# Performance work log

Measured on AMD Instinct MI355X. Metric: run time of the kernel, lower is better.

## Reference

```python
import jax, jax.numpy as jnp
import numpy as np

N_NODES = 50000
N_EDGES = 800000
IN_FEATS = 96
HIDDEN = 96
OUT_FEATS = 8


def setup_inputs() -> dict:
    key = jax.random.key(0)
    k = jax.random.split(key, 10)
    features = jax.random.normal(k[0], (N_NODES, IN_FEATS), dtype=jnp.float32)
    src = jax.random.randint(k[1], (N_EDGES,), 0, N_NODES, dtype=jnp.int32)
    dst = jax.random.randint(k[2], (N_EDGES,), 0, N_NODES, dtype=jnp.int32)
    # DGL GraphConv weights: shape (in, out), xavier-uniform; bias zeros (we use small randn for nontrivial grads)
    def glorot(kk, fan_in, fan_out):
        lim = np.sqrt(6.0 / (fan_in + fan_out))
        return jax.random.uniform(kk, (fan_in, fan_out), jnp.float32, -lim, lim)
    W1 = glorot(k[3], IN_FEATS, HIDDEN)
    b1 = jnp.zeros((HIDDEN,), jnp.float32)
    W2 = glorot(k[4], HIDDEN, HIDDEN)
    b2 = jnp.zeros((HIDDEN,), jnp.float32)
    # torch Linear readout: weight [out, in], bias [out]
    Wr = glorot(k[5], OUT_FEATS, HIDDEN)
    br = jnp.zeros((OUT_FEATS,), jnp.float32)
    return {"features": features, "src": src, "dst": dst,
            "W1": W1, "b1": b1, "W2": W2, "b2": b2, "Wr": Wr, "br": br}


def _degree_norms(src, dst, n_nodes):
    ones = jnp.ones(src.shape[0], jnp.float32)
    deg_out = jax.ops.segment_sum(ones, src, num_segments=n_nodes)
    deg_in = jax.ops.segment_sum(ones, dst, num_segments=n_nodes)
    norm_out = jnp.clip(deg_out, 1.0, None) ** -0.5  # D_out^{-1/2}
    norm_in = jnp.clip(deg_in, 1.0, None) ** -0.5    # D_in^{-1/2}
    return norm_out, norm_in


def _graph_conv(x, src, dst, norm_out, norm_in, W, b):
    # DGL GraphConv, norm='both': scale src feats, sum-aggregate over edges,
    # scale by in-degree norm, dense transform + bias.
    x = x * norm_out[:, None]
    msgs = x[src]                                           # [E, d] gather
    agg = jax.ops.segment_sum(msgs, dst, num_segments=x.shape[0])  # [N, d] scatter-add
    agg = agg * norm_in[:, None]
    return agg @ W + b


def reference(features, src, dst, W1, b1, W2, b2, Wr, br):
    n = features.shape[0]
    norm_out, norm_in = _degree_norms(src, dst, n)
    x = jax.nn.relu(_graph_conv(features, src, dst, norm_out, norm_in, W1, b1))
    x = _graph_conv(x, src, dst, norm_out, norm_in, W2, b2)
    hg = jnp.mean(x, axis=0, keepdims=True)  # [1, hidden]
    return hg @ Wr.T + br                    # [1, out_feats]
```

## Files before the change

### kernel.cpp

```cpp
#include <hip/hip_runtime.h>


constexpr int NN = 50000;
constexpr int NE = 800000;
constexpr int NB = 196;
constexpr int CAP = 6144;

constexpr int OFF_SVEC     = 0;
constexpr int OFF_BCURD    = 256;
constexpr int OFF_BCURS    = 3392;
constexpr int OFF_NORM_OUT = 6528;
constexpr int OFF_NORM_IN  = 56528;
constexpr int OFF_CW       = 106528;
constexpr int OFF_ROW_PTR  = 156528;
constexpr int OFF_EDGE_SRC = 206532;
constexpr int OFF_PD       = 606532;
constexpr int OFF_PS       = 1810756;
constexpr int OFF_YP       = 606532;
constexpr size_t ZERO_BYTES = (size_t)(OFF_NORM_OUT) * 4;

__global__ __launch_bounds__(256)
void k_part(const int* __restrict__ src, const int* __restrict__ dst,
            int* __restrict__ bcur_d, int* __restrict__ bcur_s,
            int* __restrict__ pd, int* __restrict__ ps) {
  __shared__ int hd[256], hs[256], cd[256], cs[256];
  const int t = threadIdx.x;
  hd[t] = 0; hs[t] = 0;
  __syncthreads();
  const int e0 = blockIdx.x * 2048;
  int s_[8], d_[8];
#pragma unroll
  for (int i = 0; i < 8; ++i) {
    int e = e0 + i * 256 + t;
    bool v = e < NE;
    s_[i] = v ? src[e] : -1;
    d_[i] = v ? dst[e] : -1;
    if (v) { atomicAdd(&hd[d_[i] >> 8], 1); atomicAdd(&hs[s_[i] >> 8], 1); }
  }
  __syncthreads();
  if (t < NB) {
    int c = hd[t];
    cd[t] = c ? (t * CAP + atomicAdd(&bcur_d[t * 16], c)) : 0;
    c = hs[t];
    cs[t] = c ? (t * CAP + atomicAdd(&bcur_s[t * 16], c)) : 0;
  }
  __syncthreads();
#pragma unroll
  for (int i = 0; i < 8; ++i) {
    if (s_[i] >= 0) {
      int pos = atomicAdd(&cd[d_[i] >> 8], 1);
      pd[pos] = (s_[i] << 8) | (d_[i] & 255);
      int pos2 = atomicAdd(&cs[s_[i] >> 8], 1);
      ps[pos2] = (d_[i] << 8) | (s_[i] & 255);
    }
  }
}

__global__ __launch_bounds__(256)
void k_csr(const int* __restrict__ pd, const int* __restrict__ bcur_d,
           int* __restrict__ row_ptr, float* __restrict__ norm_in,
           unsigned short* __restrict__ edge_src) {
  __shared__ int hist[256], cur[256], sc[256];
  const int t = threadIdx.x, b = blockIdx.x;
  hist[t] = 0;
  __syncthreads();
  const int cnt = bcur_d[b * 16];
  const int* pe = pd + b * CAP;
  for (int i = t; i < cnt; i += 256) atomicAdd(&hist[pe[i] & 255], 1);

  sc[t] = (t < b) ? bcur_d[t * 16] : 0;
  __syncthreads();
  for (int s = 128; s > 0; s >>= 1) {
    if (t < s) sc[t] += sc[t + s];
    __syncthreads();
  }
  const int base0 = sc[0];
  __syncthreads();

  int h = hist[t];
  sc[t] = h;
  __syncthreads();
  for (int off = 1; off < 256; off <<= 1) {
    int u = (t >= off) ? sc[t - off] : 0;
    __syncthreads();
    sc[t] += u;
    __syncthreads();
  }
  int excl = base0 + sc[t] - h;
  int n = b * 256 + t;
  if (n < NN) {
    row_ptr[n] = excl;
    norm_in[n] = 1.0f / sqrtf((float)max(h, 1));
  }
  cur[t] = excl;
  __syncthreads();
  if (b == NB - 1 && t == 0) row_ptr[NN] = base0 + cnt;

  for (int i = t; i < cnt; i += 256) {
    int p = pe[i];
    int pos = atomicAdd(&cur[p & 255], 1);
    edge_src[pos] = (unsigned short)(p >> 8);
  }
}

__global__ __launch_bounds__(256)
void k_bin_src(const int* __restrict__ ps, const int* __restrict__ bcur_s,
               const float* __restrict__ norm_in,
               float* __restrict__ norm_out, float* __restrict__ cw) {
  __shared__ int dout[256];
  __shared__ float craw[256];
  const int t = threadIdx.x, b = blockIdx.x;
  dout[t] = 0; craw[t] = 0.f;
  __syncthreads();
  const int cnt = bcur_s[b * 16];
  const int* pe = ps + b * CAP;
  for (int i = t; i < cnt; i += 256) {
    int p = pe[i];
    atomicAdd(&dout[p & 255], 1);
    atomicAdd(&craw[p & 255], norm_in[p >> 8]);
  }
  __syncthreads();
  int n = b * 256 + t;
  if (n < NN) {
    float no = 1.0f / sqrtf((float)max(dout[t], 1));
    norm_out[n] = no;
    cw[n] = no * craw[t];
  }
}

__global__ __launch_bounds__(256, 6)
void k_xform(const float* __restrict__ feats, const float* __restrict__ norm_out,
             const float* __restrict__ W1, float* __restrict__ YP) {
  __shared__ float XT[96][68];
  const int t = threadIdx.x;
  const int nb = blockIdx.x * 64;

  const float4* f4 = (const float4*)feats;
#pragma unroll
  for (int i = 0; i < 6; ++i) {
    int idx4 = i * 256 + t;
    int n = idx4 / 24;
    int kq = idx4 % 24;
    int ng = nb + n;
    float4 v = make_float4(0.f, 0.f, 0.f, 0.f);
    float no = 0.f;
    if (ng < NN) { v = f4[(size_t)ng * 24 + kq]; no = norm_out[ng]; }
    XT[kq * 4 + 0][n] = v.x * no;
    XT[kq * 4 + 1][n] = v.y * no;
    XT[kq * 4 + 2][n] = v.z * no;
    XT[kq * 4 + 3][n] = v.w * no;
  }
  __syncthreads();

  const int tn = t & 7;
  const int tm = t >> 3;
  float acc0[12], acc1[12];
#pragma unroll
  for (int c = 0; c < 12; ++c) { acc0[c] = 0.f; acc1[c] = 0.f; }

  const float4* W4 = (const float4*)(W1 + 12 * tn);
#pragma unroll 4
  for (int k = 0; k < 96; ++k) {
    float2 x = *(const float2*)&XT[k][2 * tm];
    float4 w0 = W4[k * 24 + 0];
    float4 w1 = W4[k * 24 + 1];
    float4 w2 = W4[k * 24 + 2];
    const float w[12] = {w0.x, w0.y, w0.z, w0.w, w1.x, w1.y, w1.z, w1.w,
                         w2.x, w2.y, w2.z, w2.w};
#pragma unroll
    for (int c = 0; c < 12; ++c) {
      acc0[c] = fmaf(x.x, w[c], acc0[c]);
      acc1[c] = fmaf(x.y, w[c], acc1[c]);
    }
  }

  int n0 = nb + 2 * tm;
  if (n0 < NN) {
    float4* yp = (float4*)(YP + ((size_t)tn * NN + n0) * 12);
    yp[0] = make_float4(acc0[0], acc0[1], acc0[2], acc0[3]);
    yp[1] = make_float4(acc0[4], acc0[5], acc0[6], acc0[7]);
    yp[2] = make_float4(acc0[8], acc0[9], acc0[10], acc0[11]);
  }
  if (n0 + 1 < NN) {
    float4* yp = (float4*)(YP + ((size_t)tn * NN + n0 + 1) * 12);
    yp[0] = make_float4(acc1[0], acc1[1], acc1[2], acc1[3]);
    yp[1] = make_float4(acc1[4], acc1[5], acc1[6], acc1[7]);
    yp[2] = make_float4(acc1[8], acc1[9], acc1[10], acc1[11]);
  }
}

__global__ __launch_bounds__(256, 6)
void k_agg(const float* __restrict__ YP,
           const float* __restrict__ norm_in, const float* __restrict__ cw,
           const int* __restrict__ row_ptr, const unsigned short* __restrict__ edge_src,
           const float* __restrict__ b1, float* __restrict__ svec) {
  __shared__ float red[12];
  const int tid = threadIdx.x;
  if (tid < 12) red[tid] = 0.f;
  __syncthreads();

  const int panel = blockIdx.x & 7;
  const int bp    = blockIdx.x >> 3;
  const int g = tid >> 5, l = tid & 31;
  const int ei = l / 3;
  const int q  = l - 3 * ei;
  const bool act = (l < 24);

  const float* Yp = YP + (size_t)panel * NN * 12;
  float4 b4 = make_float4(0.f, 0.f, 0.f, 0.f);
  if (l < 3) b4 = ((const float4*)b1)[3 * panel + l];

  float a0 = 0.f, a1 = 0.f, a2 = 0.f, a3 = 0.f;

  const int gid = bp * 8 + g;
  for (int n = gid; n < NN; n += 4096) {
    const int m = n + 2048;
    const bool hb = (m < NN);
    int e1a = row_ptr[n + 1], basea = row_ptr[n];
    int e1b = 0, baseb = 0;
    if (hb) { e1b = row_ptr[m + 1]; baseb = row_ptr[m]; }
    float va0 = 0.f, va1 = 0.f, va2 = 0.f, va3 = 0.f;
    float vb0 = 0.f, vb1 = 0.f, vb2 = 0.f, vb3 = 0.f;

    while (basea < e1a || baseb < e1b) {
      int cnta = min(32, e1a - basea);
      int cntb = min(32, e1b - baseb);
      int esa = 0, esb = 0;
      if (basea + l < e1a) esa = edge_src[basea + l];
      if (baseb + l < e1b) esb = edge_src[baseb + l];

      if (cnta > 0) {
        int s0 = __shfl(esa, ei, 32);
        float4 f0 = make_float4(0.f, 0.f, 0.f, 0.f);
        if (act && ei < cnta) f0 = *(const float4*)(Yp + (size_t)s0 * 12 + 4 * q);
        if (cnta > 8) {
          int s1 = __shfl(esa, 8 + ei, 32);
          float4 f1 = make_float4(0.f, 0.f, 0.f, 0.f);
          if (act && 8 + ei < cnta) f1 = *(const float4*)(Yp + (size_t)s1 * 12 + 4 * q);
          f0.x += f1.x; f0.y += f1.y; f0.z += f1.z; f0.w += f1.w;
        }
        if (cnta > 16) {
          int s2 = __shfl(esa, 16 + ei, 32);
          int s3 = __shfl(esa, 24 + ei, 32);
          float4 f2 = make_float4(0.f, 0.f, 0.f, 0.f), f3 = f2;
          if (act && 16 + ei < cnta) f2 = *(const float4*)(Yp + (size_t)s2 * 12 + 4 * q);
          if (act && 24 + ei < cnta) f3 = *(const float4*)(Yp + (size_t)s3 * 12 + 4 * q);
          f0.x += f2.x + f3.x; f0.y += f2.y + f3.y;
          f0.z += f2.z + f3.z; f0.w += f2.w + f3.w;
        }
        va0 += f0.x; va1 += f0.y; va2 += f0.z; va3 += f0.w;
      }
      if (cntb > 0) {
        int s0 = __shfl(esb, ei, 32);
        float4 f0 = make_float4(0.f, 0.f, 0.f, 0.f);
        if (act && ei < cntb) f0 = *(const float4*)(Yp + (size_t)s0 * 12 + 4 * q);
        if (cntb > 8) {
          int s1 = __shfl(esb, 8 + ei, 32);
          float4 f1 = make_float4(0.f, 0.f, 0.f, 0.f);
          if (act && 8 + ei < cntb) f1 = *(const float4*)(Yp + (size_t)s1 * 12 + 4 * q);
          f0.x += f1.x; f0.y += f1.y; f0.z += f1.z; f0.w += f1.w;
        }
        if (cntb > 16) {
          int s2 = __shfl(esb, 16 + ei, 32);
          int s3 = __shfl(esb, 24 + ei, 32);
          float4 f2 = make_float4(0.f, 0.f, 0.f, 0.f), f3 = f2;
          if (act && 16 + ei < cntb) f2 = *(const float4*)(Yp + (size_t)s2 * 12 + 4 * q);
          if (act && 24 + ei < cntb) f3 = *(const float4*)(Yp + (size_t)s3 * 12 + 4 * q);
          f0.x += f2.x + f3.x; f0.y += f2.y + f3.y;
          f0.z += f2.z + f3.z; f0.w += f2.w + f3.w;
        }
        vb0 += f0.x; vb1 += f0.y; vb2 += f0.z; vb3 += f0.w;
      }
      basea += 32; baseb += 32;
    }

    va0 += __shfl(va0, l + 12, 32); va1 += __shfl(va1, l + 12, 32);
    va2 += __shfl(va2, l + 12, 32); va3 += __shfl(va3, l + 12, 32);
    va0 += __shfl(va0, l + 6, 32);  va1 += __shfl(va1, l + 6, 32);
    va2 += __shfl(va2, l + 6, 32);  va3 += __shfl(va3, l + 6, 32);
    va0 += __shfl(va0, l + 3, 32);  va1 += __shfl(va1, l + 3, 32);
    va2 += __shfl(va2, l + 3, 32);  va3 += __shfl(va3, l + 3, 32);

    vb0 += __shfl(vb0, l + 12, 32); vb1 += __shfl(vb1, l + 12, 32);
    vb2 += __shfl(vb2, l + 12, 32); vb3 += __shfl(vb3, l + 12, 32);
    vb0 += __shfl(vb0, l + 6, 32);  vb1 += __shfl(vb1, l + 6, 32);
    vb2 += __shfl(vb2, l + 6, 32);  vb3 += __shfl(vb3, l + 6, 32);
    vb0 += __shfl(vb0, l + 3, 32);  vb1 += __shfl(vb1, l + 3, 32);
    vb2 += __shfl(vb2, l + 3, 32);  vb3 += __shfl(vb3, l + 3, 32);

    if (l < 3) {
      float ni = norm_in[n], c = cw[n];
      a0 += c * fmaxf(fmaf(ni, va0, b4.x), 0.f);
      a1 += c * fmaxf(fmaf(ni, va1, b4.y), 0.f);
      a2 += c * fmaxf(fmaf(ni, va2, b4.z), 0.f);
      a3 += c * fmaxf(fmaf(ni, va3, b4.w), 0.f);
      if (hb) {
        float nib = norm_in[m], cb = cw[m];
        a0 += cb * fmaxf(fmaf(nib, vb0, b4.x), 0.f);
        a1 += cb * fmaxf(fmaf(nib, vb1, b4.y), 0.f);
        a2 += cb * fmaxf(fmaf(nib, vb2, b4.z), 0.f);
        a3 += cb * fmaxf(fmaf(nib, vb3, b4.w), 0.f);
      }
    }
  }

  if (l < 3) {
    atomicAdd(&red[4 * l + 0], a0);
    atomicAdd(&red[4 * l + 1], a1);
    atomicAdd(&red[4 * l + 2], a2);
    atomicAdd(&red[4 * l + 3], a3);
  }
  __syncthreads();
  if (tid < 12) atomicAdd(&svec[12 * panel + tid], red[tid]);
}

__global__ void k_final(const float* __restrict__ svec,
                        const float* __restrict__ W2, const float* __restrict__ b2,
                        const float* __restrict__ Wr, const float* __restrict__ br,
                        float* __restrict__ out) {
  __shared__ float hg[96];
  int j = threadIdx.x;
  if (j < 96) {
    float acc = b2[j];
    const float invN = 1.0f / (float)NN;
    for (int k = 0; k < 96; ++k)
      acc = fmaf(svec[k] * invN, W2[k * 96 + j], acc);
    hg[j] = acc;
  }
  __syncthreads();
  if (j < 8) {
    float acc = br[j];
    for (int k = 0; k < 96; ++k)
      acc = fmaf(hg[k], Wr[j * 96 + k], acc);
    out[j] = acc;
  }
}

extern "C" void kernel_launch(void* const* d_in, const int* in_sizes, int n_in,
                              void* d_out, int out_size, void* d_ws, size_t ws_size,
                              hipStream_t stream) {
  const float* feats = (const float*)d_in[0];
  const int*   src   = (const int*)d_in[1];
  const int*   dst   = (const int*)d_in[2];
  const float* W1    = (const float*)d_in[3];
  const float* b1    = (const float*)d_in[4];
  const float* W2    = (const float*)d_in[5];
  const float* b2    = (const float*)d_in[6];
  const float* Wr    = (const float*)d_in[7];
  const float* br    = (const float*)d_in[8];
  float* out = (float*)d_out;

  int*   wsi      = (int*)d_ws;
  float* wsf      = (float*)d_ws;
  float* svec     = wsf + OFF_SVEC;
  int*   bcur_d   = wsi + OFF_BCURD;
  int*   bcur_s   = wsi + OFF_BCURS;
  float* norm_out = wsf + OFF_NORM_OUT;
  float* norm_in  = wsf + OFF_NORM_IN;
  float* cw       = wsf + OFF_CW;
  int*   row_ptr  = wsi + OFF_ROW_PTR;
  unsigned short* edge_src = (unsigned short*)(wsi + OFF_EDGE_SRC);
  int*   pd       = wsi + OFF_PD;
  int*   ps       = wsi + OFF_PS;
  float* YP       = wsf + OFF_YP;

  hipMemsetAsync(d_ws, 0, ZERO_BYTES, stream);

  k_part<<<(NE + 2047) / 2048, 256, 0, stream>>>(src, dst, bcur_d, bcur_s, pd, ps);
  k_csr<<<NB, 256, 0, stream>>>(pd, bcur_d, row_ptr, norm_in, edge_src);
  k_bin_src<<<NB, 256, 0, stream>>>(ps, bcur_s, norm_in, norm_out, cw);
  k_xform<<<(NN + 63) / 64, 256, 0, stream>>>(feats, norm_out, W1, YP);
  k_agg<<<2048, 256, 0, stream>>>(YP, norm_in, cw, row_ptr, edge_src, b1, svec);
  k_final<<<1, 128, 0, stream>>>(svec, W2, b2, Wr, br, out);
}
```

Before: 226.3 us.

## Stage partition writes in LDS, cache CSR bucket in LDS, prescale gather indices

The partition kernel now sorts each block's edges by bucket in shared memory, using a local prefix scan, and then writes them to the global bucket arrays as contiguous runs. This replaces scattered per-edge atomic-slot writes and is meant to coalesce the stores. The CSR kernel keeps its bucket in shared memory so the second pass does not re-read global memory. The aggregation kernel multiplies source indices by 12 once and uses 32-bit offsets, which removes per-load 64-bit address arithmetic. In exchange, the partition kernel uses much more shared memory and adds extra syncs and scans.

New measurement: 219.5 us. 3.0% less time.

```diff
diff --git a/kernel.cpp b/kernel.cpp
--- a/kernel.cpp
+++ b/kernel.cpp
@@ -23,7 +23,10 @@
 void k_part(const int* __restrict__ src, const int* __restrict__ dst,
             int* __restrict__ bcur_d, int* __restrict__ bcur_s,
             int* __restrict__ pd, int* __restrict__ ps) {
-  __shared__ int hd[256], hs[256], cd[256], cs[256];
+  __shared__ int hd[256], hs[256], gd[256], gs[256];
+  __shared__ int ldx[256], cur[256], scn[256];
+  __shared__ int stage[2048];
+  __shared__ unsigned char stageB[2048];
   const int t = threadIdx.x;
   hd[t] = 0; hs[t] = 0;
   __syncthreads();
@@ -40,19 +43,64 @@
   __syncthreads();
   if (t < NB) {
     int c = hd[t];
-    cd[t] = c ? (t * CAP + atomicAdd(&bcur_d[t * 16], c)) : 0;
+    gd[t] = c ? (t * CAP + atomicAdd(&bcur_d[t * 16], c)) : 0;
     c = hs[t];
-    cs[t] = c ? (t * CAP + atomicAdd(&bcur_s[t * 16], c)) : 0;
-  }
+    gs[t] = c ? (t * CAP + atomicAdd(&bcur_s[t * 16], c)) : 0;
+  }
+
+  scn[t] = hd[t];
+  __syncthreads();
+  for (int off = 1; off < 256; off <<= 1) {
+    int u = (t >= off) ? scn[t - off] : 0;
+    __syncthreads();
+    scn[t] += u;
+    __syncthreads();
+  }
+  ldx[t] = scn[t] - hd[t];
+  cur[t] = scn[t] - hd[t];
+  const int totd = scn[255];
+  __syncthreads();
+#pragma unroll
+  for (int i = 0; i < 8; ++i) {
+    if (d_[i] >= 0) {
+      int B = d_[i] >> 8;
+      int p = atomicAdd(&cur[B], 1);
+      stage[p] = (s_[i] << 8) | (d_[i] & 255);
+      stageB[p] = (unsigned char)B;
+    }
+  }
+  __syncthreads();
+  for (int j = t; j < totd; j += 256) {
+    int B = stageB[j];
+    pd[gd[B] + (j - ldx[B])] = stage[j];
+  }
+  __syncthreads();
+
+  scn[t] = hs[t];
+  __syncthreads();
+  for (int off = 1; off < 256; off <<= 1) {
+    int u = (t >= off) ? scn[t - off] : 0;
+    __syncthreads();
+    scn[t] += u;
+    __syncthreads();
+  }
+  ldx[t] = scn[t] - hs[t];
+  cur[t] = scn[t] - hs[t];
+  const int tots = scn[255];
   __syncthreads();
 #pragma unroll
   for (int i = 0; i < 8; ++i) {
     if (s_[i] >= 0) {
-      int pos = atomicAdd(&cd[d_[i] >> 8], 1);
-      pd[pos] = (s_[i] << 8) | (d_[i] & 255);
-      int pos2 = atomicAdd(&cs[s_[i] >> 8], 1);
-      ps[pos2] = (d_[i] << 8) | (s_[i] & 255);
+      int B = s_[i] >> 8;
+      int p = atomicAdd(&cur[B], 1);
+      stage[p] = (d_[i] << 8) | (s_[i] & 255);
+      stageB[p] = (unsigned char)B;
     }
+  }
+  __syncthreads();
+  for (int j = t; j < tots; j += 256) {
+    int B = stageB[j];
+    ps[gs[B] + (j - ldx[B])] = stage[j];
   }
 }
 
@@ -60,13 +108,18 @@
 void k_csr(const int* __restrict__ pd, const int* __restrict__ bcur_d,
            int* __restrict__ row_ptr, float* __restrict__ norm_in,
            unsigned short* __restrict__ edge_src) {
+  __shared__ int pe_s[CAP];
   __shared__ int hist[256], cur[256], sc[256];
   const int t = threadIdx.x, b = blockIdx.x;
   hist[t] = 0;
   __syncthreads();
   const int cnt = bcur_d[b * 16];
   const int* pe = pd + b * CAP;
-  for (int i = t; i < cnt; i += 256) atomicAdd(&hist[pe[i] & 255], 1);
+  for (int i = t; i < cnt; i += 256) {
+    int p = pe[i];
+    pe_s[i] = p;
+    atomicAdd(&hist[p & 255], 1);
+  }
 
   sc[t] = (t < b) ? bcur_d[t * 16] : 0;
   __syncthreads();
@@ -97,7 +150,7 @@
   if (b == NB - 1 && t == 0) row_ptr[NN] = base0 + cnt;
 
   for (int i = t; i < cnt; i += 256) {
-    int p = pe[i];
+    int p = pe_s[i];
     int pos = atomicAdd(&cur[p & 255], 1);
     edge_src[pos] = (unsigned short)(p >> 8);
   }
@@ -203,7 +256,7 @@
   const int bp    = blockIdx.x >> 3;
   const int g = tid >> 5, l = tid & 31;
   const int ei = l / 3;
-  const int q  = l - 3 * ei;
+  const int q4 = (l - 3 * ei) * 4;
   const bool act = (l < 24);
 
   const float* Yp = YP + (size_t)panel * NN * 12;
@@ -226,25 +279,25 @@
       int cnta = min(32, e1a - basea);
       int cntb = min(32, e1b - baseb);
       int esa = 0, esb = 0;
-      if (basea + l < e1a) esa = edge_src[basea + l];
-      if (baseb + l < e1b) esb = edge_src[baseb + l];
+      if (basea + l < e1a) esa = edge_src[basea + l] * 12;
+      if (baseb + l < e1b) esb = edge_src[baseb + l] * 12;
 
       if (cnta > 0) {
         int s0 = __shfl(esa, ei, 32);
         float4 f0 = make_float4(0.f, 0.f, 0.f, 0.f);
-        if (act && ei < cnta) f0 = *(const float4*)(Yp + (size_t)s0 * 12 + 4 * q);
+        if (act && ei < cnta) f0 = *(const float4*)(Yp + s0 + q4);
         if (cnta > 8) {
           int s1 = __shfl(esa, 8 + ei, 32);
           float4 f1 = make_float4(0.f, 0.f, 0.f, 0.f);
-          if (act && 8 + ei < cnta) f1 = *(const float4*)(Yp + (size_t)s1 * 12 + 4 * q);
+          if (act && 8 + ei < cnta) f1 = *(const float4*)(Yp + s1 + q4);
           f0.x += f1.x; f0.y += f1.y; f0.z += f1.z; f0.w += f1.w;
         }
         if (cnta > 16) {
           int s2 = __shfl(esa, 16 + ei, 32);
           int s3 = __shfl(esa, 24 + ei, 32);
           float4 f2 = make_float4(0.f, 0.f, 0.f, 0.f), f3 = f2;
-          if (act && 16 + ei < cnta) f2 = *(const float4*)(Yp + (size_t)s2 * 12 + 4 * q);
-          if (act && 24 + ei < cnta) f3 = *(const float4*)(Yp + (size_t)s3 * 12 + 4 * q);
+          if (act && 16 + ei < cnta) f2 = *(const float4*)(Yp + s2 + q4);
+          if (act && 24 + ei < cnta) f3 = *(const float4*)(Yp + s3 + q4);
           f0.x += f2.x + f3.x; f0.y += f2.y + f3.y;
           f0.z += f2.z + f3.z; f0.w += f2.w + f3.w;
         }
@@ -253,19 +306,19 @@
       if (cntb > 0) {
         int s0 = __shfl(esb, ei, 32);
         float4 f0 = make_float4(0.f, 0.f, 0.f, 0.f);
-        if (act && ei < cntb) f0 = *(const float4*)(Yp + (size_t)s0 * 12 + 4 * q);
+        if (act && ei < cntb) f0 = *(const float4*)(Yp + s0 + q4);
         if (cntb > 8) {
           int s1 = __shfl(esb, 8 + ei, 32);
           float4 f1 = make_float4(0.f, 0.f, 0.f, 0.f);
-          if (act && 8 + ei < cntb) f1 = *(const float4*)(Yp + (size_t)s1 * 12 + 4 * q);
+          if (act && 8 + ei < cntb) f1 = *(const float4*)(Yp + s1 + q4);
           f0.x += f1.x; f0.y += f1.y; f0.z += f1.z; f0.w += f1.w;
         }
         if (cntb > 16) {
           int s2 = __shfl(esb, 16 + ei, 32);
           int s3 = __shfl(esb, 24 + ei, 32);
           float4 f2 = make_float4(0.f, 0.f, 0.f, 0.f), f3 = f2;
-          if (act && 16 + ei < cntb) f2 = *(const float4*)(Yp + (size_t)s2 * 12 + 4 * q);
-          if (act && 24 + ei < cntb) f3 = *(const float4*)(Yp + (size_t)s3 * 12 + 4 * q);
+          if (act && 16 + ei < cntb) f2 = *(const float4*)(Yp + s2 + q4);
+          if (act && 24 + ei < cntb) f3 = *(const float4*)(Yp + s3 + q4);
           f0.x += f2.x + f3.x; f0.y += f2.y + f3.y;
           f0.z += f2.z + f3.z; f0.w += f2.w + f3.w;
         }
```
